# Kernel optimization log

Measured on AMD Instinct MI355X. Metric: run time of the kernel, lower is better.

Reference implementation:

```python
import jax, jax.numpy as jnp
import numpy as np

B, S, D, H = 8, 1024, 1024, 16
HD = D // H
EPS = 1e-06


def setup_inputs() -> dict:
    key = jax.random.key(0)
    ks = jax.random.split(key, 10)
    sc = 0.02
    inp = {
        "y": jax.random.normal(ks[0], (B, S, D), dtype=jnp.float32),
        "y_mask": jax.random.randint(ks[1], (B, 1, 1, S), 0, 2) == 1,
        "Wq": jax.random.normal(ks[2], (D, D), dtype=jnp.float32) * sc,
        "bq": jnp.zeros((D,), jnp.float32),
        "Wk": jax.random.normal(ks[3], (D, D), dtype=jnp.float32) * sc,
        "bk": jnp.zeros((D,), jnp.float32),
        "Wv": jax.random.normal(ks[4], (D, D), dtype=jnp.float32) * sc,
        "bv": jnp.zeros((D,), jnp.float32),
        "Wm": jax.random.normal(ks[5], (D, D), dtype=jnp.float32) * sc,
        "bm": jnp.zeros((D,), jnp.float32),
        "a2": jnp.ones((D,), jnp.float32),
        "b2": jnp.zeros((D,), jnp.float32),
    }
    return inp


def _heads(x):
    # [B,S,D] -> [B,H,S,HD]
    return x.reshape(B, S, H, HD).transpose(0, 2, 1, 3)


def reference(y, y_mask, Wq, bq, Wk, bk, Wv, bv, Wm, bm, a2, b2):
    # torch Linear: x @ W^T + b
    q = _heads(y @ Wq.T + bq)
    k = _heads(y @ Wk.T + bk)
    v = _heads(y @ Wv.T + bv)
    scores = jnp.einsum("bhqd,bhkd->bhqk", q, k) / jnp.sqrt(jnp.float32(HD))
    scores = jnp.where(y_mask, jnp.float32(-1e9), scores)
    att = jax.nn.softmax(scores, axis=-1)  # dropout = identity in eval
    atted = jnp.einsum("bhqk,bhkd->bhqd", att, v)
    atted = atted.transpose(0, 2, 1, 3).reshape(B, S, D)
    atted = atted @ Wm.T + bm
    x = y + atted  # residual (dropout1 = identity in eval)
    mean = x.mean(-1, keepdims=True)
    # torch std: unbiased (ddof=1); eps added to std, not variance
    std = jnp.sqrt(((x - mean) ** 2).sum(-1, keepdims=True) / jnp.float32(D - 1))
    return a2 * (x - mean) / (std + EPS) + b2
```

## Files before the change

### kernel.cpp

```cpp
#include <hip/hip_runtime.h>

#define DEVFN __device__ __forceinline__

typedef unsigned short u16;
typedef __attribute__((ext_vector_type(8))) unsigned short u16x8;
typedef __attribute__((ext_vector_type(4))) unsigned short u16x4;
typedef __attribute__((ext_vector_type(8))) __bf16 bf16x8;
typedef __attribute__((ext_vector_type(4))) float f32x4;

DEVFN u16 f2bf_hw(float f) {
    return __builtin_bit_cast(u16, (__bf16)f);
}

DEVFN float bf2f(u16 h) {
    unsigned u = (unsigned)h << 16;
    return __builtin_bit_cast(float, u);
}

DEVFN bf16x8 ldfrag(const u16* p) {
    return __builtin_bit_cast(bf16x8, *(const u16x8*)p);
}

DEVFN f32x4 mfma16(bf16x8 a, bf16x8 b, f32x4 c) {
    return __builtin_amdgcn_mfma_f32_16x16x32_bf16(a, b, c, 0, 0, 0);
}

DEVFN void async16(const u16* g, u16* l) {
    __builtin_amdgcn_global_load_lds(
        (const __attribute__((address_space(1))) void*)g,
        (__attribute__((address_space(3))) void*)l, 16, 0, 0);
}

__global__ __launch_bounds__(256) void conv_all(const float* __restrict__ y,
                                                const float* __restrict__ w0,
                                                const float* __restrict__ w1,
                                                const float* __restrict__ w2,
                                                const float* __restrict__ w3,
                                                u16* __restrict__ yb,
                                                u16* __restrict__ wb,
                                                const int* __restrict__ mask,
                                                int* __restrict__ idx,
                                                int* __restrict__ cnt) {
    const int b = blockIdx.x;
    if (b >= 12288) {
        const int wave = threadIdx.x >> 6, lane = threadIdx.x & 63;
        for (int bb = wave; bb < 8; bb += 4) {
            const int* m = mask + bb * 1024;
            int* ib = idx + bb * 1024;
            int base = 0;
            for (int t = 0; t < 16; ++t) {
                const int pos = t * 64 + lane;
                const int valid = (m[pos] == 0) ? 1 : 0;
                const unsigned long long bal = __ballot(valid);
                const int pre = __popcll(bal & ((1ull << lane) - 1ull));
                if (valid) ib[base + pre] = pos;
                base += (int)__popcll(bal);
            }
            if (lane == 0) cnt[bb] = base;
            for (int i = base + lane; i < 1024; i += 64) ib[i] = 0;
        }
        return;
    }
    const float* src;
    u16* dst;
    int i;
    if (b < 8192) {
        src = y; dst = yb;
        i = b * 1024 + threadIdx.x * 4;
    } else {
        const int g = (b - 8192) >> 10;
        src = g == 0 ? w0 : (g == 1 ? w1 : (g == 2 ? w2 : w3));
        dst = wb + (size_t)g * 1024 * 1024;
        i = ((b - 8192) & 1023) * 1024 + threadIdx.x * 4;
    }
    const float4 v = *(const float4*)&src[i];
    u16x4 o;
    o.x = f2bf_hw(v.x); o.y = f2bf_hw(v.y);
    o.z = f2bf_hw(v.z); o.w = f2bf_hw(v.w);
    *(u16x4*)&dst[i] = o;
}

__global__ __launch_bounds__(256, 4) void gemm_bt(const u16* __restrict__ A,
                                                  const u16* __restrict__ Bt,
                                                  const float* __restrict__ b0,
                                                  const float* __restrict__ b1,
                                                  const float* __restrict__ b2,
                                                  u16* __restrict__ C0,
                                                  u16* __restrict__ C1,
                                                  u16* __restrict__ C2,
                                                  int K) {
    __shared__ u16 lA[128 * 32];
    __shared__ u16 lB[128 * 32];
    const int tid = threadIdx.x;
    const int wave = tid >> 6, lane = tid & 63;
    const int quad = lane >> 4, l16 = lane & 15;
    const int n0 = blockIdx.x * 128, m0 = blockIdx.y * 128;
    const int wm = (wave >> 1) * 64, wn = (wave & 1) * 64;
    const int srow = tid >> 2, scol = (tid & 3) * 8;
    const u16* Ag0 = A + (size_t)(m0 + srow) * K + scol;
    const u16* Ag1 = A + (size_t)(m0 + 64 + srow) * K + scol;
    const u16* Bg0 = Bt + (size_t)(n0 + srow) * K + scol;
    const u16* Bg1 = Bt + (size_t)(n0 + 64 + srow) * K + scol;
    u16* lA0 = &lA[wave * 512];
    u16* lA1 = &lA[2048 + wave * 512];
    u16* lB0 = &lB[wave * 512];
    u16* lB1 = &lB[2048 + wave * 512];
    f32x4 acc[4][4] = {};
    for (int k0 = 0; k0 < K; k0 += 32) {
        __syncthreads();
        async16(Ag0 + k0, lA0);
        async16(Ag1 + k0, lA1);
        async16(Bg0 + k0, lB0);
        async16(Bg1 + k0, lB1);
        __syncthreads();
        bf16x8 af[4], bfr[4];
        #pragma unroll
        for (int i = 0; i < 4; ++i)
            af[i] = ldfrag(&lA[(wm + i * 16 + l16) * 32 + quad * 8]);
        #pragma unroll
        for (int i = 0; i < 4; ++i)
            bfr[i] = ldfrag(&lB[(wn + i * 16 + l16) * 32 + quad * 8]);
        #pragma unroll
        for (int mi = 0; mi < 4; ++mi)
            #pragma unroll
            for (int ni = 0; ni < 4; ++ni)
                acc[mi][ni] = mfma16(af[mi], bfr[ni], acc[mi][ni]);
    }
    #pragma unroll
    for (int mi = 0; mi < 4; ++mi) {
        #pragma unroll
        for (int ni = 0; ni < 4; ++ni) {
            const int col = n0 + wn + ni * 16 + l16;
            const int cs = col >> 10;
            const int c = col & 1023;
            const float* bp = cs == 0 ? b0 : (cs == 1 ? b1 : b2);
            u16* cp = cs == 0 ? C0 : (cs == 1 ? C1 : C2);
            const float bb = bp[c];
            #pragma unroll
            for (int r = 0; r < 4; ++r) {
                const int row = m0 + wm + mi * 16 + quad * 4 + r;
                cp[(size_t)row * 1024 + c] = f2bf_hw(acc[mi][ni][r] + bb);
            }
        }
    }
}

__global__ __launch_bounds__(256) void attn(const u16* __restrict__ qb,
                                            const u16* __restrict__ kb,
                                            const u16* __restrict__ vb,
                                            const int* __restrict__ idxb,
                                            const int* __restrict__ cntb,
                                            u16* __restrict__ attb) {
    const int lin = blockIdx.x;
    const int xcd = lin & 7, slot = lin >> 3;
    const int bh = xcd * 16 + (slot >> 3);
    const int q0 = (slot & 7) * 128;
    const int bb = bh >> 4, h = bh & 15;
    const int tid = threadIdx.x, wave = tid >> 6, lane = tid & 63;
    const int quad = lane >> 4, l16 = lane & 15;
    __shared__ u16 lK[64 * 72];
    __shared__ u16 lV[64 * 72];
    __shared__ u16 lP[128 * 72];

    const int cn = cntb[bb];
    const int kEnd = (cn + 63) & ~63;
    const int* ib = idxb + bb * 1024;

    bf16x8 aq[2][2];
    #pragma unroll
    for (int rg = 0; rg < 2; ++rg) {
        const int qrow = q0 + wave * 32 + rg * 16 + l16;
        const u16* qp = qb + (size_t)(bb * 1024 + qrow) * 1024 + h * 64 + quad * 8;
        aq[rg][0] = ldfrag(qp);
        aq[rg][1] = ldfrag(qp + 32);
    }

    f32x4 o[2][4] = {};
    float ps_acc[2][4] = {};

    const int srow = tid >> 3, scol = (tid & 7) * 8;
    const u16* kbase = kb + (size_t)(bb * 1024) * 1024 + h * 64 + scol;
    const u16* vbase = vb + (size_t)(bb * 1024) * 1024 + h * 64 + scol;

    int gi0 = ib[srow], gi1 = ib[srow + 32];
    u16x8 nk0 = *(const u16x8*)(kbase + (size_t)gi0 * 1024);
    u16x8 nk1 = *(const u16x8*)(kbase + (size_t)gi1 * 1024);
    u16x8 nv0 = *(const u16x8*)(vbase + (size_t)gi0 * 1024);
    u16x8 nv1 = *(const u16x8*)(vbase + (size_t)gi1 * 1024);

    const float C = 0.18033688011112043f;

    for (int kt = 0; kt < kEnd; kt += 64) {
        __syncthreads();
        *(u16x8*)&lK[srow * 72 + scol] = nk0;
        *(u16x8*)&lK[(srow + 32) * 72 + scol] = nk1;
        #pragma unroll
        for (int j = 0; j < 8; ++j) {
            lV[(scol + j) * 72 + srow] = nv0[j];
            lV[(scol + j) * 72 + srow + 32] = nv1[j];
        }
        __syncthreads();
        const int ktn = kt + 64;
        if (ktn < kEnd) {
            gi0 = ib[ktn + srow]; gi1 = ib[ktn + srow + 32];
            nk0 = *(const u16x8*)(kbase + (size_t)gi0 * 1024);
            nk1 = *(const u16x8*)(kbase + (size_t)gi1 * 1024);
            nv0 = *(const u16x8*)(vbase + (size_t)gi0 * 1024);
            nv1 = *(const u16x8*)(vbase + (size_t)gi1 * 1024);
        }

        bf16x8 kf[4][2];
        #pragma unroll
        for (int n = 0; n < 4; ++n) {
            kf[n][0] = ldfrag(&lK[(n * 16 + l16) * 72 + quad * 8]);
            kf[n][1] = ldfrag(&lK[(n * 16 + l16) * 72 + 32 + quad * 8]);
        }
        f32x4 s[2][4];
        #pragma unroll
        for (int rg = 0; rg < 2; ++rg)
            #pragma unroll
            for (int n = 0; n < 4; ++n) {
                f32x4 t = {};
                t = mfma16(aq[rg][0], kf[n][0], t);
                t = mfma16(aq[rg][1], kf[n][1], t);
                s[rg][n] = t;
            }
        float bias[4];
        #pragma unroll
        for (int n = 0; n < 4; ++n)
            bias[n] = (kt + n * 16 + l16 < cn) ? 0.0f : -1e9f;
        #pragma unroll
        for (int rg = 0; rg < 2; ++rg)
            #pragma unroll
            for (int n = 0; n < 4; ++n)
                #pragma unroll
                for (int r = 0; r < 4; ++r) {
                    const float p =
                        __builtin_amdgcn_exp2f(__builtin_fmaf(s[rg][n][r], C, bias[n]));
                    ps_acc[rg][r] += p;
                    lP[(wave * 32 + rg * 16 + quad * 4 + r) * 72 + n * 16 + l16] =
                        f2bf_hw(p);
                }
        __asm__ __volatile__("s_waitcnt lgkmcnt(0)" ::: "memory");
        bf16x8 ap[2][2];
        #pragma unroll
        for (int rg = 0; rg < 2; ++rg) {
            ap[rg][0] = ldfrag(&lP[(wave * 32 + rg * 16 + l16) * 72 + quad * 8]);
            ap[rg][1] = ldfrag(&lP[(wave * 32 + rg * 16 + l16) * 72 + 32 + quad * 8]);
        }
        bf16x8 vf[4][2];
        #pragma unroll
        for (int ni = 0; ni < 4; ++ni) {
            vf[ni][0] = ldfrag(&lV[(ni * 16 + l16) * 72 + quad * 8]);
            vf[ni][1] = ldfrag(&lV[(ni * 16 + l16) * 72 + 32 + quad * 8]);
        }
        #pragma unroll
        for (int rg = 0; rg < 2; ++rg)
            #pragma unroll
            for (int ni = 0; ni < 4; ++ni) {
                o[rg][ni] = mfma16(ap[rg][0], vf[ni][0], o[rg][ni]);
                o[rg][ni] = mfma16(ap[rg][1], vf[ni][1], o[rg][ni]);
            }
    }
    #pragma unroll
    for (int off = 1; off < 16; off <<= 1)
        #pragma unroll
        for (int rg = 0; rg < 2; ++rg)
            #pragma unroll
            for (int r = 0; r < 4; ++r)
                ps_acc[rg][r] += __shfl_xor(ps_acc[rg][r], off);
    float rl[2][4];
    #pragma unroll
    for (int rg = 0; rg < 2; ++rg)
        #pragma unroll
        for (int r = 0; r < 4; ++r) rl[rg][r] = 1.f / ps_acc[rg][r];
    #pragma unroll
    for (int rg = 0; rg < 2; ++rg)
        #pragma unroll
        for (int ni = 0; ni < 4; ++ni)
            #pragma unroll
            for (int r = 0; r < 4; ++r) {
                const int row = q0 + wave * 32 + rg * 16 + quad * 4 + r;
                attb[(size_t)(bb * 1024 + row) * 1024 + h * 64 + ni * 16 + l16] =
                    f2bf_hw(o[rg][ni][r] * rl[rg][r]);
            }
}

__global__ __launch_bounds__(256) void ln_res(const u16* __restrict__ ybf,
                                              const u16* __restrict__ xpb,
                                              const float* __restrict__ a2,
                                              const float* __restrict__ b2,
                                              float* __restrict__ out) {
    const int row = blockIdx.x, tid = threadIdx.x;
    const size_t base = (size_t)row * 1024;
    const int j = tid * 4;
    const u16x4 yv = *(const u16x4*)&ybf[base + j];
    const u16x4 xv = *(const u16x4*)&xpb[base + j];
    float x[4] = {bf2f(yv.x) + bf2f(xv.x), bf2f(yv.y) + bf2f(xv.y),
                  bf2f(yv.z) + bf2f(xv.z), bf2f(yv.w) + bf2f(xv.w)};
    float s = 0.f, ss = 0.f;
    #pragma unroll
    for (int i = 0; i < 4; ++i) { s += x[i]; ss += x[i] * x[i]; }
    #pragma unroll
    for (int off = 1; off < 64; off <<= 1) {
        s += __shfl_xor(s, off);
        ss += __shfl_xor(ss, off);
    }
    __shared__ float rs[4], rss[4];
    const int wave = tid >> 6, lane = tid & 63;
    if (lane == 0) { rs[wave] = s; rss[wave] = ss; }
    __syncthreads();
    s = rs[0] + rs[1] + rs[2] + rs[3];
    ss = rss[0] + rss[1] + rss[2] + rss[3];
    const float mean = s * (1.f / 1024.f);
    float var = (ss - s * mean) * (1.f / 1023.f);
    var = fmaxf(var, 0.f);
    const float inv = 1.f / (sqrtf(var) + 1e-6f);
    const float4 av = *(const float4*)&a2[j];
    const float4 bv = *(const float4*)&b2[j];
    float4 ov;
    ov.x = av.x * (x[0] - mean) * inv + bv.x;
    ov.y = av.y * (x[1] - mean) * inv + bv.y;
    ov.z = av.z * (x[2] - mean) * inv + bv.z;
    ov.w = av.w * (x[3] - mean) * inv + bv.w;
    *(float4*)&out[base + j] = ov;
}

extern "C" void kernel_launch(void* const* d_in, const int* in_sizes, int n_in,
                              void* d_out, int out_size, void* d_ws, size_t ws_size,
                              hipStream_t stream) {
    (void)in_sizes; (void)n_in; (void)out_size;
    const float* y   = (const float*)d_in[0];
    const int*   msk = (const int*)d_in[1];
    const float* Wq  = (const float*)d_in[2];
    const float* bq  = (const float*)d_in[3];
    const float* Wk  = (const float*)d_in[4];
    const float* bkb = (const float*)d_in[5];
    const float* Wv  = (const float*)d_in[6];
    const float* bv  = (const float*)d_in[7];
    const float* Wm  = (const float*)d_in[8];
    const float* bm  = (const float*)d_in[9];
    const float* a2  = (const float*)d_in[10];
    const float* b2  = (const float*)d_in[11];
    float* out = (float*)d_out;

    char* ws = (char*)d_ws;
    const size_t MB = 1u << 20;
    if (ws_size < 72 * MB) return;
    u16* yb  = (u16*)(ws);
    u16* wqb = (u16*)(ws + 16 * MB);
    u16* wmb = (u16*)(ws + 22 * MB);
    u16* qb  = (u16*)(ws + 24 * MB);
    u16* kb  = (u16*)(ws + 40 * MB);
    u16* vb  = (u16*)(ws + 56 * MB);
    u16* xpb  = qb;

    int* idxb = (int*)d_out;
    int* cntb = idxb + 8192;
    u16* attb = (u16*)((char*)d_out + 16 * MB);

    conv_all<<<12289, 256, 0, stream>>>(y, Wq, Wk, Wv, Wm, yb, wqb,
                                        msk, idxb, cntb);

    gemm_bt<<<dim3(24, 64), 256, 0, stream>>>(
        yb, wqb, bq, bkb, bv, qb, kb, vb, 1024);

    attn<<<dim3(1024), 256, 0, stream>>>(qb, kb, vb, idxb, cntb, attb);

    gemm_bt<<<dim3(8, 64), 256, 0, stream>>>(
        attb, wmb, bm, bm, bm, xpb, xpb, xpb, 1024);

    ln_res<<<8192, 256, 0, stream>>>(yb, xpb, a2, b2, out);
}
```

Measured before the change: 277.3 us.

## Add 256x256 eight-wave pipelined GEMM for fused QKV projection

Adds a new gemm8_bt kernel that computes the fused QKV projection with 256x256 tiles, 512 threads and a double-buffered async global-to-LDS pipeline. LDS reads and MFMA phases are interleaved with barriers and s_setprio, and workgroups are remapped across XCDs. The aim is more data reuse per tile and better overlap of loads with matrix math than the old 128x128 kernel. In exchange it uses more LDS and registers per block, and the grid is only 384 blocks, which limits occupancy and hurts tail balance.

```diff
diff --git a/kernel.cpp b/kernel.cpp
--- a/kernel.cpp
+++ b/kernel.cpp
@@ -78,6 +78,158 @@
     o.x = f2bf_hw(v.x); o.y = f2bf_hw(v.y);
     o.z = f2bf_hw(v.z); o.w = f2bf_hw(v.w);
     *(u16x4*)&dst[i] = o;
+}
+
+__global__ __launch_bounds__(512, 2) void gemm8_bt(const u16* __restrict__ A,
+                                                   const u16* __restrict__ Bt,
+                                                   const float* __restrict__ b0,
+                                                   const float* __restrict__ b1,
+                                                   const float* __restrict__ b2,
+                                                   u16* __restrict__ C0,
+                                                   u16* __restrict__ C1,
+                                                   u16* __restrict__ C2,
+                                                   int K, int NBX) {
+    __shared__ u16 lds[2][2][2][8192];
+    const int NT = K >> 6;
+    const int tid = threadIdx.x;
+    const int wave = tid >> 6, lane = tid & 63;
+    const int quad = lane >> 4, l16 = lane & 15;
+    const int wm = wave >> 2;
+    const int wn = wave & 3;
+    const int nwg = gridDim.x;
+    const int cpx = nwg >> 3;
+    const int sb = (blockIdx.x & 7) * cpx + (blockIdx.x >> 3);
+    const int bx = sb % NBX, by = sb / NBX;
+    const int m0 = by * 256, n0 = bx * 256;
+    const int sr = lane >> 3, sc = lane & 7;
+    const int scs = ((sc ^ sr) << 3);
+    const u16* Ag = A + (size_t)(m0 + wave * 8 + sr) * K + scs;
+    const u16* Bg = Bt + (size_t)(n0 + wave * 8 + sr) * K + scs;
+    const size_t hstep = (size_t)128 * K;
+    const int rof = l16 * 64 + ((quad ^ (l16 & 7)) << 3);
+    const int nioff = (wn & 1) * 4096;
+
+#define STAGE(gptr, lptr)                                  \
+    do {                                                   \
+        async16((gptr), (lptr) + wave * 512);              \
+        async16((gptr) + (size_t)64 * K,                   \
+                (lptr) + 4096 + wave * 512);               \
+    } while (0)
+
+    f32x4 acc[8][4] = {};
+
+    STAGE(Bg, &lds[0][1][0][0]);
+    STAGE(Ag, &lds[0][0][0][0]);
+    STAGE(Bg + hstep, &lds[0][1][1][0]);
+    STAGE(Ag + hstep, &lds[0][0][1][0]);
+    STAGE(Bg + 64, &lds[1][1][0][0]);
+    STAGE(Ag + 64, &lds[1][0][0][0]);
+    STAGE(Bg + hstep + 64, &lds[1][1][1][0]);
+    asm volatile("s_waitcnt vmcnt(6)" ::: "memory");
+    __builtin_amdgcn_s_barrier();
+
+    for (int t = 0; t < NT; ++t) {
+        const int buf = t & 1;
+        const u16* Ar = &lds[buf][0][wm][0];
+        const u16* Br = &lds[buf][1][wn >> 1][0] + nioff;
+        bf16x8 af[4][2], bfr[4][2];
+        #pragma unroll
+        for (int mi = 0; mi < 4; ++mi) {
+            af[mi][0] = ldfrag(Ar + mi * 1024 + rof);
+            af[mi][1] = ldfrag(Ar + mi * 1024 + (rof ^ 32));
+        }
+        #pragma unroll
+        for (int ni = 0; ni < 2; ++ni) {
+            bfr[ni][0] = ldfrag(Br + ni * 1024 + rof);
+            bfr[ni][1] = ldfrag(Br + ni * 1024 + (rof ^ 32));
+        }
+        if (t + 1 < NT)
+            STAGE(Ag + hstep + (size_t)(t + 1) * 64, &lds[buf ^ 1][0][1][0]);
+        __builtin_amdgcn_s_barrier();
+        asm volatile("s_waitcnt lgkmcnt(0)" ::: "memory");
+        __builtin_amdgcn_s_setprio(1);
+        #pragma unroll
+        for (int mi = 0; mi < 4; ++mi)
+            #pragma unroll
+            for (int ni = 0; ni < 2; ++ni) {
+                acc[mi][ni] = mfma16(af[mi][0], bfr[ni][0], acc[mi][ni]);
+                acc[mi][ni] = mfma16(af[mi][1], bfr[ni][1], acc[mi][ni]);
+            }
+        __builtin_amdgcn_s_setprio(0);
+        __builtin_amdgcn_s_barrier();
+        #pragma unroll
+        for (int ni = 2; ni < 4; ++ni) {
+            bfr[ni][0] = ldfrag(Br + ni * 1024 + rof);
+            bfr[ni][1] = ldfrag(Br + ni * 1024 + (rof ^ 32));
+        }
+        __builtin_amdgcn_s_barrier();
+        asm volatile("s_waitcnt lgkmcnt(0)" ::: "memory");
+        __builtin_amdgcn_s_setprio(1);
+        #pragma unroll
+        for (int mi = 0; mi < 4; ++mi)
+            #pragma unroll
+            for (int ni = 2; ni < 4; ++ni) {
+                acc[mi][ni] = mfma16(af[mi][0], bfr[ni][0], acc[mi][ni]);
+                acc[mi][ni] = mfma16(af[mi][1], bfr[ni][1], acc[mi][ni]);
+            }
+        __builtin_amdgcn_s_setprio(0);
+        __builtin_amdgcn_s_barrier();
+        #pragma unroll
+        for (int mi = 0; mi < 4; ++mi) {
+            af[mi][0] = ldfrag(Ar + (mi + 4) * 1024 + rof);
+            af[mi][1] = ldfrag(Ar + (mi + 4) * 1024 + (rof ^ 32));
+        }
+        if (t + 2 < NT)
+            STAGE(Bg + (size_t)(t + 2) * 64, &lds[buf][1][0][0]);
+        __builtin_amdgcn_s_barrier();
+        asm volatile("s_waitcnt lgkmcnt(0)" ::: "memory");
+        __builtin_amdgcn_s_setprio(1);
+        #pragma unroll
+        for (int mi = 0; mi < 4; ++mi)
+            #pragma unroll
+            for (int ni = 0; ni < 2; ++ni) {
+                acc[mi + 4][ni] = mfma16(af[mi][0], bfr[ni][0], acc[mi + 4][ni]);
+                acc[mi + 4][ni] = mfma16(af[mi][1], bfr[ni][1], acc[mi + 4][ni]);
+            }
+        __builtin_amdgcn_s_setprio(0);
+        __builtin_amdgcn_s_barrier();
+        if (t + 2 < NT) {
+            STAGE(Ag + (size_t)(t + 2) * 64, &lds[buf][0][0][0]);
+            STAGE(Bg + hstep + (size_t)(t + 2) * 64, &lds[buf][1][1][0]);
+        }
+        __builtin_amdgcn_s_setprio(1);
+        #pragma unroll
+        for (int mi = 0; mi < 4; ++mi)
+            #pragma unroll
+            for (int ni = 2; ni < 4; ++ni) {
+                acc[mi + 4][ni] = mfma16(af[mi][0], bfr[ni][0], acc[mi + 4][ni]);
+                acc[mi + 4][ni] = mfma16(af[mi][1], bfr[ni][1], acc[mi + 4][ni]);
+            }
+        __builtin_amdgcn_s_setprio(0);
+        if (t < NT - 2)
+            asm volatile("s_waitcnt vmcnt(6)" ::: "memory");
+        else
+            asm volatile("s_waitcnt vmcnt(0)" ::: "memory");
+        __builtin_amdgcn_s_barrier();
+    }
+#undef STAGE
+    const int wmrow = m0 + wm * 128 + quad * 4;
+    #pragma unroll
+    for (int ni = 0; ni < 4; ++ni) {
+        const int col = n0 + wn * 64 + ni * 16 + l16;
+        const int cs = col >> 10;
+        const int c = col & 1023;
+        const float* bp = cs == 0 ? b0 : (cs == 1 ? b1 : b2);
+        u16* cp = cs == 0 ? C0 : (cs == 1 ? C1 : C2);
+        const float bb = bp[c];
+        #pragma unroll
+        for (int mi = 0; mi < 8; ++mi)
+            #pragma unroll
+            for (int r = 0; r < 4; ++r) {
+                const int row = wmrow + mi * 16 + r;
+                cp[(size_t)row * 1024 + c] = f2bf_hw(acc[mi][ni][r] + bb);
+            }
+    }
 }
 
 __global__ __launch_bounds__(256, 4) void gemm_bt(const u16* __restrict__ A,
@@ -362,8 +514,8 @@
     conv_all<<<12289, 256, 0, stream>>>(y, Wq, Wk, Wv, Wm, yb, wqb,
                                         msk, idxb, cntb);
 
-    gemm_bt<<<dim3(24, 64), 256, 0, stream>>>(
-        yb, wqb, bq, bkb, bv, qb, kb, vb, 1024);
+    gemm8_bt<<<dim3(384), 512, 0, stream>>>(
+        yb, wqb, bq, bkb, bv, qb, kb, vb, 1024, 12);
 
     attn<<<dim3(1024), 256, 0, stream>>>(qb, kb, vb, idxb, cntb, attb);
 
```

New measurement: 279.0 us. About the same (+0.6%).

## Rewrite projection GEMM as double-buffered 256x128 tile with swizzled LDS

Applied to the files above, without the earlier changes.

The bf16 GEMM used for the QKV and output projections is replaced by an 8-wave 256x128-tile kernel with K-step 64. It double-buffers LDS with async global-to-LDS loads issued between the two MFMA halves and XOR-swizzles the LDS layout to avoid bank conflicts. It also remaps block IDs so consecutive tiles land on the same XCD and raises MFMA wave priority. This is meant to hide global load latency and improve reuse compared with the single-buffered 128x128 K=32 loop. The cost is more LDS per block (96KB), lower occupancy, and hand-written waitcnt/barrier logic that must be exactly right.

```diff
diff --git a/kernel.cpp b/kernel.cpp
--- a/kernel.cpp
+++ b/kernel.cpp
@@ -80,68 +80,121 @@
     *(u16x4*)&dst[i] = o;
 }
 
-__global__ __launch_bounds__(256, 4) void gemm_bt(const u16* __restrict__ A,
-                                                  const u16* __restrict__ Bt,
-                                                  const float* __restrict__ b0,
-                                                  const float* __restrict__ b1,
-                                                  const float* __restrict__ b2,
-                                                  u16* __restrict__ C0,
-                                                  u16* __restrict__ C1,
-                                                  u16* __restrict__ C2,
-                                                  int K) {
-    __shared__ u16 lA[128 * 32];
-    __shared__ u16 lB[128 * 32];
+__global__ __launch_bounds__(512, 2) void gemm8b(const u16* __restrict__ A,
+                                                 const u16* __restrict__ Bt,
+                                                 const float* __restrict__ b0,
+                                                 const float* __restrict__ b1,
+                                                 const float* __restrict__ b2,
+                                                 u16* __restrict__ C0,
+                                                 u16* __restrict__ C1,
+                                                 u16* __restrict__ C2,
+                                                 int K, int NBX) {
+    __shared__ u16 lds[2][24576];
+    const int NT = K >> 6;
     const int tid = threadIdx.x;
     const int wave = tid >> 6, lane = tid & 63;
     const int quad = lane >> 4, l16 = lane & 15;
-    const int n0 = blockIdx.x * 128, m0 = blockIdx.y * 128;
-    const int wm = (wave >> 1) * 64, wn = (wave & 1) * 64;
-    const int srow = tid >> 2, scol = (tid & 3) * 8;
-    const u16* Ag0 = A + (size_t)(m0 + srow) * K + scol;
-    const u16* Ag1 = A + (size_t)(m0 + 64 + srow) * K + scol;
-    const u16* Bg0 = Bt + (size_t)(n0 + srow) * K + scol;
-    const u16* Bg1 = Bt + (size_t)(n0 + 64 + srow) * K + scol;
-    u16* lA0 = &lA[wave * 512];
-    u16* lA1 = &lA[2048 + wave * 512];
-    u16* lB0 = &lB[wave * 512];
-    u16* lB1 = &lB[2048 + wave * 512];
+    const int wm = wave >> 1, wn = wave & 1;
+    const int nwg = gridDim.x, cpx = nwg >> 3;
+    const int sb = (blockIdx.x & 7) * cpx + (blockIdx.x >> 3);
+    const int bx = sb % NBX, by = sb / NBX;
+    const int m0 = by * 256, n0 = bx * 128;
+    const int sr = lane >> 3, sc = lane & 7;
+    const int scs = (sc ^ sr) << 3;
+    const u16* Ag = A + (size_t)(m0 + wave * 8 + sr) * K + scs;
+    const u16* Bg = Bt + (size_t)(n0 + wave * 8 + sr) * K + scs;
+    const size_t rstep = (size_t)64 * K;
+    const int swz = (quad ^ (l16 & 7)) << 3;
+    const int rofA = (wm * 64 + l16) * 64 + swz;
+    const int rofB = (wn * 64 + l16) * 64 + swz;
+
+#define STAGE(gp, lp)                                        \
+    do {                                                     \
+        async16((gp), (lp) + wave * 512);                    \
+        async16((gp) + rstep, (lp) + 4096 + wave * 512);     \
+    } while (0)
+
     f32x4 acc[4][4] = {};
-    for (int k0 = 0; k0 < K; k0 += 32) {
-        __syncthreads();
-        async16(Ag0 + k0, lA0);
-        async16(Ag1 + k0, lA1);
-        async16(Bg0 + k0, lB0);
-        async16(Bg1 + k0, lB1);
-        __syncthreads();
-        bf16x8 af[4], bfr[4];
-        #pragma unroll
-        for (int i = 0; i < 4; ++i)
-            af[i] = ldfrag(&lA[(wm + i * 16 + l16) * 32 + quad * 8]);
-        #pragma unroll
-        for (int i = 0; i < 4; ++i)
-            bfr[i] = ldfrag(&lB[(wn + i * 16 + l16) * 32 + quad * 8]);
+
+    STAGE(Ag, &lds[0][0]);
+    STAGE(Ag + 2 * rstep, &lds[0][8192]);
+    STAGE(Bg, &lds[0][16384]);
+    STAGE(Ag + 64, &lds[1][0]);
+    STAGE(Ag + 2 * rstep + 64, &lds[1][8192]);
+    asm volatile("s_waitcnt vmcnt(4)" ::: "memory");
+    __builtin_amdgcn_s_barrier();
+
+    for (int t = 0; t < NT; ++t) {
+        const int buf = t & 1;
+        const u16* Ar = &lds[buf][0];
+        const u16* Br = &lds[buf][16384];
+        bf16x8 af[4][2], bfr[4][2];
+        #pragma unroll
+        for (int mi = 0; mi < 4; ++mi) {
+            af[mi][0] = ldfrag(Ar + mi * 1024 + rofA);
+            af[mi][1] = ldfrag(Ar + mi * 1024 + (rofA ^ 32));
+        }
+        #pragma unroll
+        for (int ni = 0; ni < 2; ++ni) {
+            bfr[ni][0] = ldfrag(Br + ni * 1024 + rofB);
+            bfr[ni][1] = ldfrag(Br + ni * 1024 + (rofB ^ 32));
+        }
+        if (t + 1 < NT) STAGE(Bg + (t + 1) * 64, &lds[buf ^ 1][16384]);
+        __builtin_amdgcn_s_barrier();
+        asm volatile("s_waitcnt lgkmcnt(0)" ::: "memory");
+        __builtin_amdgcn_s_setprio(1);
         #pragma unroll
         for (int mi = 0; mi < 4; ++mi)
             #pragma unroll
-            for (int ni = 0; ni < 4; ++ni)
-                acc[mi][ni] = mfma16(af[mi], bfr[ni], acc[mi][ni]);
-    }
-    #pragma unroll
-    for (int mi = 0; mi < 4; ++mi) {
-        #pragma unroll
-        for (int ni = 0; ni < 4; ++ni) {
-            const int col = n0 + wn + ni * 16 + l16;
-            const int cs = col >> 10;
-            const int c = col & 1023;
-            const float* bp = cs == 0 ? b0 : (cs == 1 ? b1 : b2);
-            u16* cp = cs == 0 ? C0 : (cs == 1 ? C1 : C2);
-            const float bb = bp[c];
+            for (int ni = 0; ni < 2; ++ni) {
+                acc[mi][ni] = mfma16(af[mi][0], bfr[ni][0], acc[mi][ni]);
+                acc[mi][ni] = mfma16(af[mi][1], bfr[ni][1], acc[mi][ni]);
+            }
+        __builtin_amdgcn_s_setprio(0);
+        __builtin_amdgcn_s_barrier();
+        #pragma unroll
+        for (int ni = 2; ni < 4; ++ni) {
+            bfr[ni][0] = ldfrag(Br + ni * 1024 + rofB);
+            bfr[ni][1] = ldfrag(Br + ni * 1024 + (rofB ^ 32));
+        }
+        if (t + 2 < NT) {
+            STAGE(Ag + (t + 2) * 64, &lds[buf][0]);
+            STAGE(Ag + 2 * rstep + (t + 2) * 64, &lds[buf][8192]);
+        }
+        __builtin_amdgcn_s_barrier();
+        asm volatile("s_waitcnt lgkmcnt(0)" ::: "memory");
+        __builtin_amdgcn_s_setprio(1);
+        #pragma unroll
+        for (int mi = 0; mi < 4; ++mi)
+            #pragma unroll
+            for (int ni = 2; ni < 4; ++ni) {
+                acc[mi][ni] = mfma16(af[mi][0], bfr[ni][0], acc[mi][ni]);
+                acc[mi][ni] = mfma16(af[mi][1], bfr[ni][1], acc[mi][ni]);
+            }
+        __builtin_amdgcn_s_setprio(0);
+        if (t < NT - 2)
+            asm volatile("s_waitcnt vmcnt(4)" ::: "memory");
+        else
+            asm volatile("s_waitcnt vmcnt(0)" ::: "memory");
+        __builtin_amdgcn_s_barrier();
+    }
+#undef STAGE
+    const int wrow = m0 + wm * 64 + quad * 4;
+    #pragma unroll
+    for (int ni = 0; ni < 4; ++ni) {
+        const int col = n0 + wn * 64 + ni * 16 + l16;
+        const int cs = col >> 10;
+        const int c = col & 1023;
+        const float* bp = cs == 0 ? b0 : (cs == 1 ? b1 : b2);
+        u16* cp = cs == 0 ? C0 : (cs == 1 ? C1 : C2);
+        const float bb = bp[c];
+        #pragma unroll
+        for (int mi = 0; mi < 4; ++mi)
             #pragma unroll
             for (int r = 0; r < 4; ++r) {
-                const int row = m0 + wm + mi * 16 + quad * 4 + r;
+                const int row = wrow + mi * 16 + r;
                 cp[(size_t)row * 1024 + c] = f2bf_hw(acc[mi][ni][r] + bb);
             }
-        }
     }
 }
 
@@ -362,13 +415,13 @@
     conv_all<<<12289, 256, 0, stream>>>(y, Wq, Wk, Wv, Wm, yb, wqb,
                                         msk, idxb, cntb);
 
-    gemm_bt<<<dim3(24, 64), 256, 0, stream>>>(
-        yb, wqb, bq, bkb, bv, qb, kb, vb, 1024);
+    gemm8b<<<dim3(768), 512, 0, stream>>>(
+        yb, wqb, bq, bkb, bv, qb, kb, vb, 1024, 24);
 
     attn<<<dim3(1024), 256, 0, stream>>>(qb, kb, vb, idxb, cntb, attb);
 
-    gemm_bt<<<dim3(8, 64), 256, 0, stream>>>(
-        attb, wmb, bm, bm, bm, xpb, xpb, xpb, 1024);
+    gemm8b<<<dim3(256), 512, 0, stream>>>(
+        attb, wmb, bm, bm, bm, xpb, xpb, xpb, 1024, 8);
 
     ln_res<<<8192, 256, 0, stream>>>(yb, xpb, a2, b2, out);
 }
```

Result: no change. 272.4 us (-1.7%).

## Compute K/V only for unmasked keys, double-buffer and swizzle GEMM LDS

Applied to the files above, without the earlier changes.

The QKV GEMM becomes a specialised kernel. Q tiles are computed densely, while K/V tiles gather only the unmasked key rows through the index list and skip tiles past the per-batch count. Attention then reads the compacted K/V contiguously instead of gathering. The GEMM main loop also gains a two-stage async LDS double buffer with explicit waitcnt and barriers, plus an XOR swizzle on LDS columns to reduce bank conflicts. The output projection reuses the same kernel with 512 blocks, and it relies on the conv kernel's index and count data being correct.

```diff
diff --git a/kernel.cpp b/kernel.cpp
--- a/kernel.cpp
+++ b/kernel.cpp
@@ -80,52 +80,94 @@
     *(u16x4*)&dst[i] = o;
 }
 
-__global__ __launch_bounds__(256, 4) void gemm_bt(const u16* __restrict__ A,
-                                                  const u16* __restrict__ Bt,
-                                                  const float* __restrict__ b0,
-                                                  const float* __restrict__ b1,
-                                                  const float* __restrict__ b2,
-                                                  u16* __restrict__ C0,
-                                                  u16* __restrict__ C1,
-                                                  u16* __restrict__ C2,
-                                                  int K) {
-    __shared__ u16 lA[128 * 32];
-    __shared__ u16 lB[128 * 32];
+__global__ __launch_bounds__(256, 4) void gemm_qkv(const u16* __restrict__ A,
+                                                   const u16* __restrict__ Wq,
+                                                   const u16* __restrict__ Wkv,
+                                                   const float* __restrict__ bq,
+                                                   const float* __restrict__ bk,
+                                                   const float* __restrict__ bv,
+                                                   u16* __restrict__ qb,
+                                                   u16* __restrict__ kb,
+                                                   u16* __restrict__ vb,
+                                                   const int* __restrict__ idxb,
+                                                   const int* __restrict__ cntb) {
+    const int K = 1024;
+    __shared__ u16 lA[2][128 * 32];
+    __shared__ u16 lB[2][128 * 32];
     const int tid = threadIdx.x;
     const int wave = tid >> 6, lane = tid & 63;
     const int quad = lane >> 4, l16 = lane & 15;
-    const int n0 = blockIdx.x * 128, m0 = blockIdx.y * 128;
     const int wm = (wave >> 1) * 64, wn = (wave & 1) * 64;
-    const int srow = tid >> 2, scol = (tid & 3) * 8;
-    const u16* Ag0 = A + (size_t)(m0 + srow) * K + scol;
-    const u16* Ag1 = A + (size_t)(m0 + 64 + srow) * K + scol;
+    const int srow = tid >> 2;
+    const int scol = (((tid & 3) ^ ((srow >> 1) & 3))) * 8;
+    const int item = blockIdx.x;
+    int m0, n0, rowbase = 0;
+    const u16* Bt;
+    const float *bp0, *bp1;
+    u16 *cp0, *cp1;
+    const int* ib = nullptr;
+    if (item < 512) {
+        m0 = (item >> 3) * 128;
+        n0 = (item & 7) * 128;
+        Bt = Wq; bp0 = bq; bp1 = bq; cp0 = qb; cp1 = qb;
+    } else {
+        const int t = item - 512;
+        const int b = t >> 7, rem = t & 127;
+        const int mb = rem >> 4, nb = rem & 15;
+        const int cn = cntb[b];
+        m0 = mb * 128;
+        if (m0 >= cn) return;
+        n0 = nb * 128;
+        rowbase = b * 1024;
+        ib = idxb + b * 1024;
+        Bt = Wkv; bp0 = bk; bp1 = bv; cp0 = kb; cp1 = vb;
+    }
+    int r0 = m0 + srow, r1 = m0 + 64 + srow;
+    if (ib) { r0 = ib[r0]; r1 = ib[r1]; }
+    const u16* Ag0 = A + (size_t)(rowbase + r0) * K + scol;
+    const u16* Ag1 = A + (size_t)(rowbase + r1) * K + scol;
     const u16* Bg0 = Bt + (size_t)(n0 + srow) * K + scol;
     const u16* Bg1 = Bt + (size_t)(n0 + 64 + srow) * K + scol;
-    u16* lA0 = &lA[wave * 512];
-    u16* lA1 = &lA[2048 + wave * 512];
-    u16* lB0 = &lB[wave * 512];
-    u16* lB1 = &lB[2048 + wave * 512];
+    const int sl = (quad ^ ((l16 >> 1) & 3)) * 8;
+
+#define STAGE(kof, bf)                                     \
+    do {                                                   \
+        async16(Ag0 + (kof), &lA[bf][wave * 512]);         \
+        async16(Ag1 + (kof), &lA[bf][2048 + wave * 512]);  \
+        async16(Bg0 + (kof), &lB[bf][wave * 512]);         \
+        async16(Bg1 + (kof), &lB[bf][2048 + wave * 512]);  \
+    } while (0)
+
     f32x4 acc[4][4] = {};
-    for (int k0 = 0; k0 < K; k0 += 32) {
-        __syncthreads();
-        async16(Ag0 + k0, lA0);
-        async16(Ag1 + k0, lA1);
-        async16(Bg0 + k0, lB0);
-        async16(Bg1 + k0, lB1);
-        __syncthreads();
+
+    STAGE(0, 0);
+    STAGE(32, 1);
+    asm volatile("s_waitcnt vmcnt(4)" ::: "memory");
+    __builtin_amdgcn_s_barrier();
+
+    for (int t = 0; t < 32; ++t) {
+        const int buf = t & 1;
         bf16x8 af[4], bfr[4];
         #pragma unroll
         for (int i = 0; i < 4; ++i)
-            af[i] = ldfrag(&lA[(wm + i * 16 + l16) * 32 + quad * 8]);
+            af[i] = ldfrag(&lA[buf][(wm + i * 16 + l16) * 32 + sl]);
         #pragma unroll
         for (int i = 0; i < 4; ++i)
-            bfr[i] = ldfrag(&lB[(wn + i * 16 + l16) * 32 + quad * 8]);
+            bfr[i] = ldfrag(&lB[buf][(wn + i * 16 + l16) * 32 + sl]);
         #pragma unroll
         for (int mi = 0; mi < 4; ++mi)
             #pragma unroll
             for (int ni = 0; ni < 4; ++ni)
                 acc[mi][ni] = mfma16(af[mi], bfr[ni], acc[mi][ni]);
-    }
+        __builtin_amdgcn_s_barrier();
+        if (t + 2 < 32) STAGE((t + 2) * 32, buf);
+        if (t < 30)
+            asm volatile("s_waitcnt vmcnt(4)" ::: "memory");
+        else
+            asm volatile("s_waitcnt vmcnt(0)" ::: "memory");
+        __builtin_amdgcn_s_barrier();
+    }
+#undef STAGE
     #pragma unroll
     for (int mi = 0; mi < 4; ++mi) {
         #pragma unroll
@@ -133,13 +175,14 @@
             const int col = n0 + wn + ni * 16 + l16;
             const int cs = col >> 10;
             const int c = col & 1023;
-            const float* bp = cs == 0 ? b0 : (cs == 1 ? b1 : b2);
-            u16* cp = cs == 0 ? C0 : (cs == 1 ? C1 : C2);
+            const float* bp = cs == 0 ? bp0 : bp1;
+            u16* cp = cs == 0 ? cp0 : cp1;
             const float bb = bp[c];
             #pragma unroll
             for (int r = 0; r < 4; ++r) {
                 const int row = m0 + wm + mi * 16 + quad * 4 + r;
-                cp[(size_t)row * 1024 + c] = f2bf_hw(acc[mi][ni][r] + bb);
+                cp[(size_t)(rowbase + row) * 1024 + c] =
+                    f2bf_hw(acc[mi][ni][r] + bb);
             }
         }
     }
@@ -148,7 +191,6 @@
 __global__ __launch_bounds__(256) void attn(const u16* __restrict__ qb,
                                             const u16* __restrict__ kb,
                                             const u16* __restrict__ vb,
-                                            const int* __restrict__ idxb,
                                             const int* __restrict__ cntb,
                                             u16* __restrict__ attb) {
     const int lin = blockIdx.x;
@@ -164,7 +206,6 @@
 
     const int cn = cntb[bb];
     const int kEnd = (cn + 63) & ~63;
-    const int* ib = idxb + bb * 1024;
 
     bf16x8 aq[2][2];
     #pragma unroll
@@ -182,11 +223,10 @@
     const u16* kbase = kb + (size_t)(bb * 1024) * 1024 + h * 64 + scol;
     const u16* vbase = vb + (size_t)(bb * 1024) * 1024 + h * 64 + scol;
 
-    int gi0 = ib[srow], gi1 = ib[srow + 32];
-    u16x8 nk0 = *(const u16x8*)(kbase + (size_t)gi0 * 1024);
-    u16x8 nk1 = *(const u16x8*)(kbase + (size_t)gi1 * 1024);
-    u16x8 nv0 = *(const u16x8*)(vbase + (size_t)gi0 * 1024);
-    u16x8 nv1 = *(const u16x8*)(vbase + (size_t)gi1 * 1024);
+    u16x8 nk0 = *(const u16x8*)(kbase + (size_t)srow * 1024);
+    u16x8 nk1 = *(const u16x8*)(kbase + (size_t)(srow + 32) * 1024);
+    u16x8 nv0 = *(const u16x8*)(vbase + (size_t)srow * 1024);
+    u16x8 nv1 = *(const u16x8*)(vbase + (size_t)(srow + 32) * 1024);
 
     const float C = 0.18033688011112043f;
 
@@ -202,11 +242,10 @@
         __syncthreads();
         const int ktn = kt + 64;
         if (ktn < kEnd) {
-            gi0 = ib[ktn + srow]; gi1 = ib[ktn + srow + 32];
-            nk0 = *(const u16x8*)(kbase + (size_t)gi0 * 1024);
-            nk1 = *(const u16x8*)(kbase + (size_t)gi1 * 1024);
-            nv0 = *(const u16x8*)(vbase + (size_t)gi0 * 1024);
-            nv1 = *(const u16x8*)(vbase + (size_t)gi1 * 1024);
+            nk0 = *(const u16x8*)(kbase + (size_t)(ktn + srow) * 1024);
+            nk1 = *(const u16x8*)(kbase + (size_t)(ktn + srow + 32) * 1024);
+            nv0 = *(const u16x8*)(vbase + (size_t)(ktn + srow) * 1024);
+            nv1 = *(const u16x8*)(vbase + (size_t)(ktn + srow + 32) * 1024);
         }
 
         bf16x8 kf[4][2];
@@ -362,13 +401,13 @@
     conv_all<<<12289, 256, 0, stream>>>(y, Wq, Wk, Wv, Wm, yb, wqb,
                                         msk, idxb, cntb);
 
-    gemm_bt<<<dim3(24, 64), 256, 0, stream>>>(
-        yb, wqb, bq, bkb, bv, qb, kb, vb, 1024);
-
-    attn<<<dim3(1024), 256, 0, stream>>>(qb, kb, vb, idxb, cntb, attb);
-
-    gemm_bt<<<dim3(8, 64), 256, 0, stream>>>(
-        attb, wmb, bm, bm, bm, xpb, xpb, xpb, 1024);
+    gemm_qkv<<<dim3(1536), 256, 0, stream>>>(
+        yb, wqb, wqb + 1024 * 1024, bq, bkb, bv, qb, kb, vb, idxb, cntb);
+
+    attn<<<dim3(1024), 256, 0, stream>>>(qb, kb, vb, cntb, attb);
+
+    gemm_qkv<<<dim3(512), 256, 0, stream>>>(
+        attb, wmb, wmb, bm, bm, bm, xpb, xpb, xpb, idxb, cntb);
 
     ln_res<<<8192, 256, 0, stream>>>(yb, xpb, a2, b2, out);
 }
```

New measurement: 268.1 us. 3.3% less time.
